# Kernel optimization log

Measured on AMD Instinct MI355X. Metric: run time of the kernel, lower is better.

Reference implementation:

```python
import jax, jax.numpy as jnp
import numpy as np

B, N, D, H = 32, 64, 256, 256
WORD_NUM, REL_NUM, POS_NUM, CAT_NUM = 50000, 50, 48, 5


def setup_inputs() -> dict:
    key = jax.random.key(0)
    ks = jax.random.split(key, 20)
    rng = np.random.default_rng(0)
    # valid dependency trees: head[i] < i, head[0] = -1 (root)
    heads_np = np.zeros((B, N), dtype=np.int32)
    for b in range(B):
        heads_np[b, 0] = -1
        for i in range(1, N):
            heads_np[b, i] = rng.integers(0, i)
    p = lambda k, shape: (0.02 * jax.random.normal(k, shape)).astype(jnp.float32)
    z = lambda shape: jnp.zeros(shape, jnp.float32)
    return {
        "xs": jax.random.randint(ks[0], (B, N), 0, WORD_NUM),
        "heads": jnp.asarray(heads_np),
        "rels": jax.random.randint(ks[1], (B, N), 0, REL_NUM),
        "labels": jax.random.randint(ks[2], (B, N), 0, WORD_NUM),
        "poss": jax.random.randint(ks[3], (B, N), 0, POS_NUM),
        "xlengths": jnp.full((B,), N, dtype=jnp.int32),
        "target_start": jnp.zeros((B,), jnp.int32),
        "target_end": jnp.full((B,), N - 1, jnp.int32),
        "x_mask": jnp.ones((B, N), jnp.float32),
        # parameters
        "emb_W": p(ks[4], (WORD_NUM, D)),
        "rel_W": p(ks[5], (REL_NUM, D)),
        "gru_Wi_f": p(ks[6], (2 * D, 3 * H)), "gru_Wh_f": p(ks[7], (H, 3 * H)),
        "gru_bi_f": z((3 * H,)), "gru_bh_f": z((3 * H,)),
        "gru_Wi_b": p(ks[8], (2 * D, 3 * H)), "gru_Wh_b": p(ks[9], (H, 3 * H)),
        "gru_bi_b": z((3 * H,)), "gru_bh_b": z((3 * H,)),
        "Wt": p(ks[10], (2 * H, D)), "bt": z((D,)),
        "dt_Wx": p(ks[11], (2 * D, 3 * H)), "dt_Uh": p(ks[12], (H, 3 * H)), "dt_b": z((3 * H,)),
        "td_Wx": p(ks[13], (2 * D, 3 * H)), "td_Uh": p(ks[14], (H, 3 * H)), "td_b": z((3 * H,)),
        "fc_W": p(ks[15], (2 * H, 100)), "fc_b": z((100,)),
        "fc2_W": p(ks[16], (100, CAT_NUM)), "fc2_b": z((CAT_NUM,)),
    }


def _gru_cell(xpt, hprev, Uh, bh):
    gh = hprev @ Uh + bh
    xr, xz, xn = jnp.split(xpt, 3, axis=-1)
    hr, hz, hn = jnp.split(gh, 3, axis=-1)
    r = jax.nn.sigmoid(xr + hr)
    zg = jax.nn.sigmoid(xz + hz)
    n = jnp.tanh(xn + r * hn)
    return (1.0 - zg) * n + zg * hprev


def _gru_dir(x, Wi, Wh, bi, bh):
    # x: [B,N,2D] -> hidden sequence [B,N,H]
    xp = x @ Wi + bi  # precompute input projections
    def step(h, xpt):
        hnew = _gru_cell(xpt, h, Wh, bh)
        return hnew, hnew
    h0 = jnp.zeros((x.shape[0], Wh.shape[0]), x.dtype)
    _, hs = jax.lax.scan(step, h0, jnp.swapaxes(xp, 0, 1))
    return jnp.swapaxes(hs, 0, 1)


def _dt_tree(inputs, heads, Wx, Uh, b):
    # bottom-up (child-sum) tree GRU; heads[b,i] < i so reversed order is topological
    Bn, Nn, _ = inputs.shape
    Hh = Uh.shape[0]
    xp = inputs @ Wx + b
    bar = jnp.arange(Bn)
    def step(carry, idx):
        C, Hout = carry  # C: accumulated child hidden sums [B,N,H]
        h = _gru_cell(xp[:, idx], C[:, idx], Uh, jnp.zeros((3 * Hh,), inputs.dtype))
        Hout = Hout.at[:, idx].set(h)
        par = heads[:, idx]
        valid = par >= 0
        C = C.at[bar, jnp.where(valid, par, 0)].add(jnp.where(valid[:, None], h, 0.0))
        return (C, Hout), None
    H0 = jnp.zeros((Bn, Nn, Hh), inputs.dtype)
    (_, Hout), _ = jax.lax.scan(step, (H0, H0), jnp.arange(Nn - 1, -1, -1))
    return Hout


def _td_tree(inputs, heads, Wx, Uh, b):
    # top-down tree GRU: parent hidden flows to children; index order 0..N-1 is topological
    Bn, Nn, _ = inputs.shape
    Hh = Uh.shape[0]
    xp = inputs @ Wx + b
    bar = jnp.arange(Bn)
    def step(Hout, idx):
        par = heads[:, idx]
        valid = par >= 0
        hp = jnp.where(valid[:, None], Hout[bar, jnp.where(valid, par, 0)], 0.0)
        h = _gru_cell(xp[:, idx], hp, Uh, jnp.zeros((3 * Hh,), inputs.dtype))
        Hout = Hout.at[:, idx].set(h)
        return Hout, None
    H0 = jnp.zeros((Bn, Nn, Hh), inputs.dtype)
    Hout, _ = jax.lax.scan(step, H0, jnp.arange(Nn))
    return Hout


def reference(xs, heads, rels, labels, poss, xlengths, target_start, target_end, x_mask,
              emb_W, rel_W,
              gru_Wi_f, gru_Wh_f, gru_bi_f, gru_bh_f,
              gru_Wi_b, gru_Wh_b, gru_bi_b, gru_bh_b,
              Wt, bt, dt_Wx, dt_Uh, dt_b, td_Wx, td_Uh, td_b,
              fc_W, fc_b, fc2_W, fc2_b):
    word_emb = emb_W[xs]
    label_emb = emb_W[labels]  # original uses self.embedding for labels too
    emb = jnp.concatenate([word_emb, label_emb], axis=-1)  # [B,N,2D]
    fwd = _gru_dir(emb, gru_Wi_f, gru_Wh_f, gru_bi_f, gru_bh_f)
    bwd = jnp.flip(_gru_dir(jnp.flip(emb, 1), gru_Wi_b, gru_Wh_b, gru_bi_b, gru_bh_b), 1)
    grus = jnp.concatenate([fwd, bwd], axis=-1) @ Wt + bt  # transform -> [B,N,D]
    rel_emb = rel_W[rels]
    outputs = jnp.concatenate([grus, rel_emb], axis=-1)  # [B,N,2D]
    dt_out = _dt_tree(outputs, heads, dt_Wx, dt_Uh, dt_b)
    td_out = _td_tree(outputs, heads, td_Wx, td_Uh, td_b)
    ctx = jnp.concatenate([dt_out, td_out], axis=-1)  # [B,N,2H]
    ctx = jnp.max(ctx, axis=1)  # max_pool1d over length -> [B,2H]
    ctx = ctx @ fc_W + fc_b
    ctx = ctx @ fc2_W + fc2_b
    return ctx
```

## Files before the change

### kernel.cpp

```cpp
#include <hip/hip_runtime.h>


typedef _Float16 half2v __attribute__((ext_vector_type(2)));
typedef _Float16 half8 __attribute__((ext_vector_type(8)));
typedef unsigned int u32x32 __attribute__((ext_vector_type(32)));
typedef float f32x4v __attribute__((ext_vector_type(4)));

__device__ __forceinline__ float fdot2f(unsigned a, unsigned b, float c) {
#if __has_builtin(__builtin_amdgcn_fdot2)
  return __builtin_amdgcn_fdot2(__builtin_bit_cast(half2v, a),
                                __builtin_bit_cast(half2v, b), c, false);
#else
  half2v av = __builtin_bit_cast(half2v, a), bv = __builtin_bit_cast(half2v, b);
  return c + (float)av.x * (float)bv.x + (float)av.y * (float)bv.y;
#endif
}

__device__ __forceinline__ unsigned packh2(float x, float y) {
  half2v p;
  p.x = (_Float16)x;
  p.y = (_Float16)y;
  return __builtin_bit_cast(unsigned, p);
}
__device__ __forceinline__ unsigned short f2u(float x) {
  return __builtin_bit_cast(unsigned short, (_Float16)x);
}
__device__ __forceinline__ float sigm(float x) { return 1.f / (1.f + __expf(-x)); }
__device__ __forceinline__ float tanh_fast(float x) {
  float cx = fminf(fmaxf(x, -15.f), 15.f);
  float e = __expf(2.f * cx);
  return (e - 1.f) / (e + 1.f);
}

__global__ __launch_bounds__(256) void pack_w(const float* __restrict__ W0,
                                              const float* __restrict__ W1,
                                              const float* __restrict__ W2,
                                              const float* __restrict__ W3, unsigned* P0,
                                              unsigned* P1, unsigned* P2, unsigned* P3) {
  const float* W;
  unsigned* P;
  switch (blockIdx.y) {
    case 0: W = W0; P = P0; break;
    case 1: W = W1; P = P1; break;
    case 2: W = W2; P = P2; break;
    default: W = W3; P = P3; break;
  }
  const int tid = blockIdx.x * 256 + threadIdx.x;
  const int i = tid & 3;
  const int u4 = tid >> 2;
  const int jg = u4 & 127;
  const int d4q = u4 >> 7;
  const int d4 = d4q % 48;
  const int q2 = d4q / 48;
  const int col2 = d4 / 24;
  const int rr = d4 % 24;
  const int g = rr >> 3;
  const int p4 = rr & 7;
  const int kp = p4 * 4 + i;
  const int k = q2 * 64 + kp * 2;
  const int col = g * 256 + col2 * 128 + jg;
  P[tid] = packh2(W[(size_t)k * 768 + col], W[(size_t)(k + 1) * 768 + col]);
}

__global__ __launch_bounds__(256) void tsplit2(const float* __restrict__ W0,
                                               const float* __restrict__ W1,
                                               unsigned short* __restrict__ H0,
                                               unsigned short* __restrict__ L0,
                                               unsigned short* __restrict__ H1,
                                               unsigned short* __restrict__ L1, int K,
                                               int N) {
  const float* __restrict__ W = blockIdx.z ? W1 : W0;
  unsigned short* __restrict__ WThi = blockIdx.z ? H1 : H0;
  unsigned short* __restrict__ WTlo = blockIdx.z ? L1 : L0;
  __shared__ float T[32][33];
  const int ky = blockIdx.y * 32, nx = blockIdx.x * 32;
  const int r = threadIdx.x >> 3, c4 = (threadIdx.x & 7) * 4;
  float4 v = *(const float4*)(W + (size_t)(ky + r) * N + nx + c4);
  T[r][c4 + 0] = v.x;
  T[r][c4 + 1] = v.y;
  T[r][c4 + 2] = v.z;
  T[r][c4 + 3] = v.w;
  __syncthreads();
  float f[4] = {T[c4 + 0][r], T[c4 + 1][r], T[c4 + 2][r], T[c4 + 3][r]};
  ushort4 oh, ol;
  {
    _Float16 h0 = (_Float16)f[0], h1 = (_Float16)f[1], h2 = (_Float16)f[2],
             h3 = (_Float16)f[3];
    oh.x = __builtin_bit_cast(unsigned short, h0);
    oh.y = __builtin_bit_cast(unsigned short, h1);
    oh.z = __builtin_bit_cast(unsigned short, h2);
    oh.w = __builtin_bit_cast(unsigned short, h3);
    ol.x = f2u(f[0] - (float)h0);
    ol.y = f2u(f[1] - (float)h1);
    ol.z = f2u(f[2] - (float)h2);
    ol.w = f2u(f[3] - (float)h3);
  }
  *(ushort4*)(WThi + (size_t)(nx + r) * K + ky + c4) = oh;
  *(ushort4*)(WTlo + (size_t)(nx + r) * K + ky + c4) = ol;
}

__global__ void gather_emb_hl(const int* __restrict__ xs, const int* __restrict__ labels,
                              const float* __restrict__ embW,
                              unsigned short* __restrict__ eHi,
                              unsigned short* __restrict__ eLo) {
  const int row = blockIdx.x, t = threadIdx.x;
  const float4* W4 = (const float4*)embW;
  const int src = (t < 64) ? xs[row] : labels[row];
  float4 v = W4[(size_t)src * 64 + (t & 63)];
  float f[4] = {v.x, v.y, v.z, v.w};
  ushort4 oh, ol;
  _Float16 h0 = (_Float16)f[0], h1 = (_Float16)f[1], h2 = (_Float16)f[2],
           h3 = (_Float16)f[3];
  oh.x = __builtin_bit_cast(unsigned short, h0);
  oh.y = __builtin_bit_cast(unsigned short, h1);
  oh.z = __builtin_bit_cast(unsigned short, h2);
  oh.w = __builtin_bit_cast(unsigned short, h3);
  ol.x = f2u(f[0] - (float)h0);
  ol.y = f2u(f[1] - (float)h1);
  ol.z = f2u(f[2] - (float)h2);
  ol.w = f2u(f[3] - (float)h3);
  const size_t idx = (size_t)row * 512 + (t >> 6) * 256 + (t & 63) * 4;
  *(ushort4*)(eHi + idx) = oh;
  *(ushort4*)(eLo + idx) = ol;
}

__global__ void gather_rel_hl(const int* __restrict__ rels,
                              const float* __restrict__ relW,
                              unsigned short* __restrict__ oHi,
                              unsigned short* __restrict__ oLo) {
  const int row = blockIdx.x, t = threadIdx.x;
  const float4* W4 = (const float4*)relW;
  float4 v = W4[(size_t)rels[row] * 64 + t];
  float f[4] = {v.x, v.y, v.z, v.w};
  ushort4 oh, ol;
  _Float16 h0 = (_Float16)f[0], h1 = (_Float16)f[1], h2 = (_Float16)f[2],
           h3 = (_Float16)f[3];
  oh.x = __builtin_bit_cast(unsigned short, h0);
  oh.y = __builtin_bit_cast(unsigned short, h1);
  oh.z = __builtin_bit_cast(unsigned short, h2);
  oh.w = __builtin_bit_cast(unsigned short, h3);
  ol.x = f2u(f[0] - (float)h0);
  ol.y = f2u(f[1] - (float)h1);
  ol.z = f2u(f[2] - (float)h2);
  ol.w = f2u(f[3] - (float)h3);
  const size_t idx = (size_t)row * 512 + 256 + t * 4;
  *(ushort4*)(oHi + idx) = oh;
  *(ushort4*)(oLo + idx) = ol;
}

__global__ __launch_bounds__(256) void mm16p2(
    const unsigned short* __restrict__ Ahi, const unsigned short* __restrict__ Alo,
    const unsigned short* __restrict__ B0h, const unsigned short* __restrict__ B0l,
    const float* __restrict__ bias0, float* __restrict__ C0,
    const unsigned short* __restrict__ B1h, const unsigned short* __restrict__ B1l,
    const float* __restrict__ bias1, float* __restrict__ C1, int ldc) {
  const unsigned short* __restrict__ Bhi = blockIdx.z ? B1h : B0h;
  const unsigned short* __restrict__ Blo = blockIdx.z ? B1l : B0l;
  const float* __restrict__ bias = blockIdx.z ? bias1 : bias0;
  float* __restrict__ Cf = blockIdx.z ? C1 : C0;
  __shared__ __align__(16) _Float16 As_h[64][40], As_l[64][40];
  __shared__ __align__(16) _Float16 Bs_h[64][40], Bs_l[64][40];
  const int t = threadIdx.x, l = t & 63, w = t >> 6;
  const int bm = blockIdx.y * 64, bn = blockIdx.x * 64;
  const int sr = t >> 2, sc = (t & 3) * 8;
  f32x4v ac0 = {0.f, 0.f, 0.f, 0.f}, ac1 = ac0, ac2 = ac0, ac3 = ac0;
  const int fr = w * 16 + (l & 15), fc = (l >> 4) * 8, lo16 = l & 15;
  for (int kt = 0; kt < 512; kt += 32) {
    *(uint4*)(&As_h[sr][sc]) = *(const uint4*)(Ahi + (size_t)(bm + sr) * 512 + kt + sc);
    *(uint4*)(&As_l[sr][sc]) = *(const uint4*)(Alo + (size_t)(bm + sr) * 512 + kt + sc);
    *(uint4*)(&Bs_h[sr][sc]) = *(const uint4*)(Bhi + (size_t)(bn + sr) * 512 + kt + sc);
    *(uint4*)(&Bs_l[sr][sc]) = *(const uint4*)(Blo + (size_t)(bn + sr) * 512 + kt + sc);
    __syncthreads();
    half8 avh = __builtin_bit_cast(half8, *(const uint4*)(&As_h[fr][fc]));
    half8 avl = __builtin_bit_cast(half8, *(const uint4*)(&As_l[fr][fc]));
#define BH(NT) __builtin_bit_cast(half8, *(const uint4*)(&Bs_h[(NT)*16 + lo16][fc]))
#define BL(NT) __builtin_bit_cast(half8, *(const uint4*)(&Bs_l[(NT)*16 + lo16][fc]))
    half8 b0h = BH(0), b1h = BH(1), b2h = BH(2), b3h = BH(3);
    half8 b0l = BL(0), b1l = BL(1), b2l = BL(2), b3l = BL(3);
#undef BH
#undef BL
    ac0 = __builtin_amdgcn_mfma_f32_16x16x32_f16(avh, b0h, ac0, 0, 0, 0);
    ac1 = __builtin_amdgcn_mfma_f32_16x16x32_f16(avh, b1h, ac1, 0, 0, 0);
    ac2 = __builtin_amdgcn_mfma_f32_16x16x32_f16(avh, b2h, ac2, 0, 0, 0);
    ac3 = __builtin_amdgcn_mfma_f32_16x16x32_f16(avh, b3h, ac3, 0, 0, 0);
    ac0 = __builtin_amdgcn_mfma_f32_16x16x32_f16(avh, b0l, ac0, 0, 0, 0);
    ac1 = __builtin_amdgcn_mfma_f32_16x16x32_f16(avh, b1l, ac1, 0, 0, 0);
    ac2 = __builtin_amdgcn_mfma_f32_16x16x32_f16(avh, b2l, ac2, 0, 0, 0);
    ac3 = __builtin_amdgcn_mfma_f32_16x16x32_f16(avh, b3l, ac3, 0, 0, 0);
    ac0 = __builtin_amdgcn_mfma_f32_16x16x32_f16(avl, b0h, ac0, 0, 0, 0);
    ac1 = __builtin_amdgcn_mfma_f32_16x16x32_f16(avl, b1h, ac1, 0, 0, 0);
    ac2 = __builtin_amdgcn_mfma_f32_16x16x32_f16(avl, b2h, ac2, 0, 0, 0);
    ac3 = __builtin_amdgcn_mfma_f32_16x16x32_f16(avl, b3h, ac3, 0, 0, 0);
    __syncthreads();
  }
  const int hi4 = l >> 4;
#define EPI(AC, NT)                                                            \
  {                                                                            \
    _Pragma("unroll") for (int i = 0; i < 4; ++i) {                            \
      const int row = bm + w * 16 + hi4 * 4 + i;                               \
      const int col = bn + (NT)*16 + lo16;                                     \
      Cf[(size_t)row * ldc + col] = (AC)[i] + bias[col];                       \
    }                                                                          \
  }
  EPI(ac0, 0) EPI(ac1, 1) EPI(ac2, 2) EPI(ac3, 3)
#undef EPI
}

__global__ __launch_bounds__(256) void mm16s_wt(const float* __restrict__ A,
                                                const float* __restrict__ W,
                                                const float* __restrict__ bias,
                                                unsigned short* __restrict__ CHi,
                                                unsigned short* __restrict__ CLo, int N,
                                                int ldc) {
  __shared__ __align__(16) _Float16 Ahi[64][40], Alo[64][40];
  __shared__ __align__(16) _Float16 Bhi[64][40], Blo[64][40];
  const int t = threadIdx.x, l = t & 63, w = t >> 6;
  const int bm = blockIdx.y * 64, bn = blockIdx.x * 64;
  const int ar = t >> 2, ac8 = (t & 3) * 8;
  const int bk = t >> 3, bn8 = (t & 7) * 8;
  f32x4v ac0 = {0.f, 0.f, 0.f, 0.f}, ac1 = ac0, ac2 = ac0, ac3 = ac0;
  const int fr = w * 16 + (l & 15), fc = (l >> 4) * 8, lo16 = l & 15;
  for (int kt = 0; kt < 512; kt += 32) {
    {
      const float* ap = A + (size_t)(bm + ar) * 512 + kt + ac8;
      float4 v0 = *(const float4*)ap;
      float4 v1 = *(const float4*)(ap + 4);
      float av[8] = {v0.x, v0.y, v0.z, v0.w, v1.x, v1.y, v1.z, v1.w};
#pragma unroll
      for (int i = 0; i < 8; ++i) {
        _Float16 h = (_Float16)av[i];
        Ahi[ar][ac8 + i] = h;
        Alo[ar][ac8 + i] = (_Float16)(av[i] - (float)h);
      }
    }
    {
      const float* wp = W + (size_t)(kt + bk) * N + bn + bn8;
      float4 v0 = *(const float4*)wp;
      float4 v1 = *(const float4*)(wp + 4);
      float wv[8] = {v0.x, v0.y, v0.z, v0.w, v1.x, v1.y, v1.z, v1.w};
#pragma unroll
      for (int i = 0; i < 8; ++i) {
        _Float16 h = (_Float16)wv[i];
        Bhi[bn8 + i][bk] = h;
        Blo[bn8 + i][bk] = (_Float16)(wv[i] - (float)h);
      }
    }
    __syncthreads();
    half8 avh = __builtin_bit_cast(half8, *(const uint4*)(&Ahi[fr][fc]));
    half8 avl = __builtin_bit_cast(half8, *(const uint4*)(&Alo[fr][fc]));
#define BH(NT) __builtin_bit_cast(half8, *(const uint4*)(&Bhi[(NT)*16 + lo16][fc]))
#define BL(NT) __builtin_bit_cast(half8, *(const uint4*)(&Blo[(NT)*16 + lo16][fc]))
    half8 b0h = BH(0), b1h = BH(1), b2h = BH(2), b3h = BH(3);
    half8 b0l = BL(0), b1l = BL(1), b2l = BL(2), b3l = BL(3);
#undef BH
#undef BL
    ac0 = __builtin_amdgcn_mfma_f32_16x16x32_f16(avh, b0h, ac0, 0, 0, 0);
    ac1 = __builtin_amdgcn_mfma_f32_16x16x32_f16(avh, b1h, ac1, 0, 0, 0);
    ac2 = __builtin_amdgcn_mfma_f32_16x16x32_f16(avh, b2h, ac2, 0, 0, 0);
    ac3 = __builtin_amdgcn_mfma_f32_16x16x32_f16(avh, b3h, ac3, 0, 0, 0);
    ac0 = __builtin_amdgcn_mfma_f32_16x16x32_f16(avh, b0l, ac0, 0, 0, 0);
    ac1 = __builtin_amdgcn_mfma_f32_16x16x32_f16(avh, b1l, ac1, 0, 0, 0);
    ac2 = __builtin_amdgcn_mfma_f32_16x16x32_f16(avh, b2l, ac2, 0, 0, 0);
    ac3 = __builtin_amdgcn_mfma_f32_16x16x32_f16(avh, b3l, ac3, 0, 0, 0);
    ac0 = __builtin_amdgcn_mfma_f32_16x16x32_f16(avl, b0h, ac0, 0, 0, 0);
    ac1 = __builtin_amdgcn_mfma_f32_16x16x32_f16(avl, b1h, ac1, 0, 0, 0);
    ac2 = __builtin_amdgcn_mfma_f32_16x16x32_f16(avl, b2h, ac2, 0, 0, 0);
    ac3 = __builtin_amdgcn_mfma_f32_16x16x32_f16(avl, b3h, ac3, 0, 0, 0);
    __syncthreads();
  }
  const int hi4 = l >> 4;
#define EPI(AC, NT)                                                            \
  {                                                                            \
    _Pragma("unroll") for (int i = 0; i < 4; ++i) {                            \
      const int row = bm + w * 16 + hi4 * 4 + i;                               \
      const int col = bn + (NT)*16 + lo16;                                     \
      float v = (AC)[i] + bias[col];                                           \
      _Float16 h = (_Float16)v;                                                \
      CHi[(size_t)row * ldc + col] = __builtin_bit_cast(unsigned short, h);    \
      CLo[(size_t)row * ldc + col] = f2u(v - (float)h);                        \
    }                                                                          \
  }
  EPI(ac0, 0) EPI(ac1, 1) EPI(ac2, 2) EPI(ac3, 3)
#undef EPI
}

template <int NP>
__device__ __forceinline__ void stage_w(const uint4* __restrict__ P4, int q2, int jg,
                                        int t, uint2 (*Wl)[512], u32x32& w0, u32x32& w1,
                                        u32x32& w2) {
#pragma unroll
  for (int p4 = 0; p4 < 8; ++p4) {
    uint4 v0 = P4[(q2 * 48 + p4) * 128 + jg];
    w0[4 * p4 + 0] = v0.x; w0[4 * p4 + 1] = v0.y;
    w0[4 * p4 + 2] = v0.z; w0[4 * p4 + 3] = v0.w;
    uint4 v1 = P4[(q2 * 48 + 8 + p4) * 128 + jg];
    w1[4 * p4 + 0] = v1.x; w1[4 * p4 + 1] = v1.y;
    w1[4 * p4 + 2] = v1.z; w1[4 * p4 + 3] = v1.w;
    uint4 v2 = P4[(q2 * 48 + 16 + p4) * 128 + jg];
    w2[4 * p4 + 0] = v2.x; w2[4 * p4 + 1] = v2.y;
    w2[4 * p4 + 2] = v2.z; w2[4 * p4 + 3] = v2.w;
  }
#pragma unroll
  for (int g = 0; g < 3; ++g)
#pragma unroll
    for (int p4 = 0; p4 < NP; ++p4) {
      uint4 v = P4[(q2 * 48 + 24 + g * 8 + p4) * 128 + jg];
      Wl[(g * NP + p4) * 2 + 0][t] = make_uint2(v.x, v.y);
      Wl[(g * NP + p4) * 2 + 1][t] = make_uint2(v.z, v.w);
    }
}

template <int NP>
__device__ __forceinline__ void dot_step(const u32x32& w0, const u32x32& w1,
                                         const u32x32& w2, const uint2 (*Wl)[512], int t,
                                         const uint4* __restrict__ P4, int sb,
                                         const uint4* hv4, float& a0, float& a1,
                                         float& a2, float& a3, float& a4, float& a5) {
#pragma unroll
  for (int c = 0; c < 8; ++c) {
    uint4 hu = hv4[c];
    a0 = fdot2f(w0[4 * c + 0], hu.x, a0); a0 = fdot2f(w0[4 * c + 1], hu.y, a0);
    a0 = fdot2f(w0[4 * c + 2], hu.z, a0); a0 = fdot2f(w0[4 * c + 3], hu.w, a0);
    a1 = fdot2f(w1[4 * c + 0], hu.x, a1); a1 = fdot2f(w1[4 * c + 1], hu.y, a1);
    a1 = fdot2f(w1[4 * c + 2], hu.z, a1); a1 = fdot2f(w1[4 * c + 3], hu.w, a1);
    a2 = fdot2f(w2[4 * c + 0], hu.x, a2); a2 = fdot2f(w2[4 * c + 1], hu.y, a2);
    a2 = fdot2f(w2[4 * c + 2], hu.z, a2); a2 = fdot2f(w2[4 * c + 3], hu.w, a2);
    if (c < NP) {
      uint2 u0 = Wl[(0 * NP + c) * 2 + 0][t], u1 = Wl[(0 * NP + c) * 2 + 1][t];
      a3 = fdot2f(u0.x, hu.x, a3); a3 = fdot2f(u0.y, hu.y, a3);
      a3 = fdot2f(u1.x, hu.z, a3); a3 = fdot2f(u1.y, hu.w, a3);
      uint2 v0 = Wl[(1 * NP + c) * 2 + 0][t], v1 = Wl[(1 * NP + c) * 2 + 1][t];
      a4 = fdot2f(v0.x, hu.x, a4); a4 = fdot2f(v0.y, hu.y, a4);
      a4 = fdot2f(v1.x, hu.z, a4); a4 = fdot2f(v1.y, hu.w, a4);
      uint2 x0 = Wl[(2 * NP + c) * 2 + 0][t], x1 = Wl[(2 * NP + c) * 2 + 1][t];
      a5 = fdot2f(x0.x, hu.x, a5); a5 = fdot2f(x0.y, hu.y, a5);
      a5 = fdot2f(x1.x, hu.z, a5); a5 = fdot2f(x1.y, hu.w, a5);
    } else {
      uint4 s0 = P4[sb + (0 * 8 + c) * 128];
      a3 = fdot2f(s0.x, hu.x, a3); a3 = fdot2f(s0.y, hu.y, a3);
      a3 = fdot2f(s0.z, hu.z, a3); a3 = fdot2f(s0.w, hu.w, a3);
      uint4 s1 = P4[sb + (1 * 8 + c) * 128];
      a4 = fdot2f(s1.x, hu.x, a4); a4 = fdot2f(s1.y, hu.y, a4);
      a4 = fdot2f(s1.z, hu.z, a4); a4 = fdot2f(s1.w, hu.w, a4);
      uint4 s2 = P4[sb + (2 * 8 + c) * 128];
      a5 = fdot2f(s2.x, hu.x, a5); a5 = fdot2f(s2.y, hu.y, a5);
      a5 = fdot2f(s2.z, hu.z, a5); a5 = fdot2f(s2.w, hu.w, a5);
    }
  }
}

__global__ __launch_bounds__(512) void gru_scan_h(
    const unsigned* __restrict__ Pf, const unsigned* __restrict__ Pb,
    const float* __restrict__ bh_f, const float* __restrict__ bh_b,
    const float* __restrict__ xp_f, const float* __restrict__ xp_b,
    float* __restrict__ grus) {
  const int b = blockIdx.x & 31, dir = blockIdx.x >> 5;
  const uint4* __restrict__ P4 = (const uint4*)(dir ? Pb : Pf);
  const float* __restrict__ bh = dir ? bh_b : bh_f;
  const float* __restrict__ xp = dir ? xp_b : xp_f;

  __shared__ uint2 Wl[36][512];
  __shared__ float part[4][3][256];
  __shared__ __align__(16) unsigned h2[128];

  const int t = threadIdx.x, jg = t & 127, q2 = t >> 7;
  const int sb = (q2 * 48 + 24) * 128 + jg;

  u32x32 w0, w1, w2;
  stage_w<6>(P4, q2, jg, t, Wl, w0, w1, w2);

  float br0 = 0.f, br1 = 0.f, bz0 = 0.f, bz1 = 0.f, bn0 = 0.f, bn1 = 0.f;
  float hp0 = 0.f, hp1 = 0.f;
  if (t < 128) {
    br0 = bh[2 * t];       br1 = bh[2 * t + 1];
    bz0 = bh[256 + 2 * t]; bz1 = bh[256 + 2 * t + 1];
    bn0 = bh[512 + 2 * t]; bn1 = bh[512 + 2 * t + 1];
    h2[t] = 0u;
  }
  __syncthreads();

  for (int s = 0; s < 64; ++s) {
    const int nn = dir ? (63 - s) : s;
    float2 pxr, pxz, pxn;
    if (t < 128) {
      const float* xrow = xp + (size_t)(b * 64 + nn) * 768;
      pxr = *(const float2*)(xrow + 2 * t);
      pxz = *(const float2*)(xrow + 256 + 2 * t);
      pxn = *(const float2*)(xrow + 512 + 2 * t);
    }
    float a0 = 0.f, a1 = 0.f, a2 = 0.f, a3 = 0.f, a4 = 0.f, a5 = 0.f;
    dot_step<6>(w0, w1, w2, Wl, t, P4, sb, (const uint4*)(h2 + q2 * 32), a0, a1, a2, a3,
                a4, a5);
    part[q2][0][jg] = a0;
    part[q2][0][128 + jg] = a3;
    part[q2][1][jg] = a1;
    part[q2][1][128 + jg] = a4;
    part[q2][2][jg] = a2;
    part[q2][2][128 + jg] = a5;
    __syncthreads();
    if (t < 128) {
      float s0r = 0, s1r = 0, s0z = 0, s1z = 0, s0n = 0, s1n = 0;
#pragma unroll
      for (int q = 0; q < 4; ++q) {
        float2 pr = *(const float2*)(&part[q][0][2 * t]); s0r += pr.x; s1r += pr.y;
        float2 pz = *(const float2*)(&part[q][1][2 * t]); s0z += pz.x; s1z += pz.y;
        float2 pn = *(const float2*)(&part[q][2][2 * t]); s0n += pn.x; s1n += pn.y;
      }
      float r0 = sigm(pxr.x + s0r + br0), r1 = sigm(pxr.y + s1r + br1);
      float z0 = sigm(pxz.x + s0z + bz0), z1 = sigm(pxz.y + s1z + bz1);
      float n0 = tanh_fast(pxn.x + r0 * (s0n + bn0));
      float n1 = tanh_fast(pxn.y + r1 * (s1n + bn1));
      float h0 = (1.f - z0) * n0 + z0 * hp0;
      float h1 = (1.f - z1) * n1 + z1 * hp1;
      hp0 = h0;
      hp1 = h1;
      h2[t] = packh2(h0, h1);
      float2 o;
      o.x = h0;
      o.y = h1;
      *(float2*)(grus + (size_t)(b * 64 + nn) * 512 + dir * 256 + 2 * t) = o;
    }
    __syncthreads();
  }
}

__global__ __launch_bounds__(512) void tree_scan_g(
    const unsigned* __restrict__ Pdt, const unsigned* __restrict__ Ptd,
    const float* __restrict__ xp_dt, const float* __restrict__ xp_td,
    const int* __restrict__ heads, float* __restrict__ ctx, float* __restrict__ Sg) {
  const int b = blockIdx.x & 31, istd = blockIdx.x >> 5;
  const uint4* __restrict__ P4 = (const uint4*)(istd ? Ptd : Pdt);
  const float* __restrict__ xp = istd ? xp_td : xp_dt;
  float* __restrict__ S = Sg + (size_t)blockIdx.x * 16384;

  __shared__ __align__(16) unsigned S2[65][128];
  __shared__ uint2 Wl[24][512];
  __shared__ float part[4][3][256];
  __shared__ int hd[64];

  const int t = threadIdx.x, jg = t & 127, q2 = t >> 7;
  const int sb = (q2 * 48 + 24) * 128 + jg;

  u32x32 w0, w1, w2;
  stage_w<4>(P4, q2, jg, t, Wl, w0, w1, w2);

  for (int i = t; i < 16384; i += 512) S[i] = 0.f;
  for (int i = t; i < 65 * 128; i += 512) (&S2[0][0])[i] = 0u;
  if (t < 64) hd[t] = heads[b * 64 + t];
  __syncthreads();

  float mx0 = -1e30f, mx1 = -1e30f;

  for (int s = 0; s < 64; ++s) {
    const int idx = istd ? s : (63 - s);
    const int par = hd[idx];
    const int srow = istd ? (par >= 0 ? par : 64) : idx;

    float2 pxr, pxz, pxn;
    float hp0 = 0.f, hp1 = 0.f, acc0 = 0.f, acc1 = 0.f;
    if (t < 128) {
      const float* xrow = xp + (size_t)(b * 64 + idx) * 768;
      pxr = *(const float2*)(xrow + 2 * t);
      pxz = *(const float2*)(xrow + 256 + 2 * t);
      pxn = *(const float2*)(xrow + 512 + 2 * t);
      if (istd) {
        if (par >= 0) {
          float2 v = *(const float2*)(S + par * 256 + 2 * t);
          hp0 = v.x;
          hp1 = v.y;
        }
      } else {
        float2 v = *(const float2*)(S + idx * 256 + 2 * t);
        hp0 = v.x;
        hp1 = v.y;
        if (par >= 0) {
          float2 a = *(const float2*)(S + par * 256 + 2 * t);
          acc0 = a.x;
          acc1 = a.y;
        }
      }
    }
    float a0 = 0.f, a1 = 0.f, a2 = 0.f, a3 = 0.f, a4 = 0.f, a5 = 0.f;
    dot_step<4>(w0, w1, w2, Wl, t, P4, sb, (const uint4*)(&S2[srow][q2 * 32]), a0, a1,
                a2, a3, a4, a5);
    part[q2][0][jg] = a0;
    part[q2][0][128 + jg] = a3;
    part[q2][1][jg] = a1;
    part[q2][1][128 + jg] = a4;
    part[q2][2][jg] = a2;
    part[q2][2][128 + jg] = a5;
    __syncthreads();
    if (t < 128) {
      float s0r = 0, s1r = 0, s0z = 0, s1z = 0, s0n = 0, s1n = 0;
#pragma unroll
      for (int q = 0; q < 4; ++q) {
        float2 pr = *(const float2*)(&part[q][0][2 * t]); s0r += pr.x; s1r += pr.y;
        float2 pz = *(const float2*)(&part[q][1][2 * t]); s0z += pz.x; s1z += pz.y;
        float2 pn = *(const float2*)(&part[q][2][2 * t]); s0n += pn.x; s1n += pn.y;
      }
      float r0 = sigm(pxr.x + s0r), r1 = sigm(pxr.y + s1r);
      float z0 = sigm(pxz.x + s0z), z1 = sigm(pxz.y + s1z);
      float n0 = tanh_fast(pxn.x + r0 * s0n), n1 = tanh_fast(pxn.y + r1 * s1n);
      float h0 = (1.f - z0) * n0 + z0 * hp0;
      float h1 = (1.f - z1) * n1 + z1 * hp1;
      mx0 = fmaxf(mx0, h0);
      mx1 = fmaxf(mx1, h1);
      if (istd) {
        float2 o;
        o.x = h0;
        o.y = h1;
        *(float2*)(S + idx * 256 + 2 * t) = o;
        S2[idx][t] = packh2(h0, h1);
      } else if (par >= 0) {
        float c0 = acc0 + h0;
        float c1 = acc1 + h1;
        float2 o;
        o.x = c0;
        o.y = c1;
        *(float2*)(S + par * 256 + 2 * t) = o;
        S2[par][t] = packh2(c0, c1);
      }
    }
    __syncthreads();
  }

  if (t < 128) {
    float2 o;
    o.x = mx0;
    o.y = mx1;
    *(float2*)(ctx + (size_t)b * 512 + istd * 256 + 2 * t) = o;
  }
}

__global__ __launch_bounds__(128) void final_k(const float* __restrict__ ctx_g,
                                               const float* __restrict__ fcW,
                                               const float* __restrict__ fcb,
                                               const float* __restrict__ fc2W,
                                               const float* __restrict__ fc2b,
                                               float* __restrict__ out) {
  const int b = blockIdx.x, t = threadIdx.x;
  __shared__ float ctx[512];
  __shared__ float f1[100];
  for (int i = t; i < 512; i += 128) ctx[i] = ctx_g[(size_t)b * 512 + i];
  __syncthreads();
  if (t < 100) {
    float a = fcb[t];
    for (int k = 0; k < 512; ++k) a = fmaf(ctx[k], fcW[k * 100 + t], a);
    f1[t] = a;
  }
  __syncthreads();
  if (t < 5) {
    float a = fc2b[t];
    for (int k = 0; k < 100; ++k) a = fmaf(f1[k], fc2W[k * 5 + t], a);
    out[b * 5 + t] = a;
  }
}

extern "C" void kernel_launch(void* const* d_in, const int* in_sizes, int n_in, void* d_out,
                              int out_size, void* d_ws, size_t ws_size, hipStream_t stream) {
  const int* xs = (const int*)d_in[0];
  const int* heads = (const int*)d_in[1];
  const int* rels = (const int*)d_in[2];
  const int* labels = (const int*)d_in[3];
  const float* emb_W = (const float*)d_in[9];
  const float* rel_W = (const float*)d_in[10];
  const float* Wi_f = (const float*)d_in[11];
  const float* Wh_f = (const float*)d_in[12];
  const float* bi_f = (const float*)d_in[13];
  const float* bh_f = (const float*)d_in[14];
  const float* Wi_b = (const float*)d_in[15];
  const float* Wh_b = (const float*)d_in[16];
  const float* bi_b = (const float*)d_in[17];
  const float* bh_b = (const float*)d_in[18];
  const float* Wt = (const float*)d_in[19];
  const float* bt = (const float*)d_in[20];
  const float* dt_Wx = (const float*)d_in[21];
  const float* dt_Uh = (const float*)d_in[22];
  const float* dt_b = (const float*)d_in[23];
  const float* td_Wx = (const float*)d_in[24];
  const float* td_Uh = (const float*)d_in[25];
  const float* td_b = (const float*)d_in[26];
  const float* fc_W = (const float*)d_in[27];
  const float* fc_b = (const float*)d_in[28];
  const float* fc2_W = (const float*)d_in[29];
  const float* fc2_b = (const float*)d_in[30];

  float* ws = (float*)d_ws;
  float* xp_f = ws;
  float* xp_b = ws + 1572864;
  float* grus = ws + 3145728;
  float* ctx = ws + 4194304;
  unsigned* P0 = (unsigned*)(ws + 4210688);
  unsigned* P1 = P0 + 98304;
  unsigned* P2 = P1 + 98304;
  unsigned* P3 = P2 + 98304;
  unsigned short* embHi = (unsigned short*)(ws + 4603904);
  unsigned short* embLo = (unsigned short*)(ws + 5128192);
  unsigned short* WTh_a = (unsigned short*)(ws + 5652480);
  unsigned short* WTl_a = (unsigned short*)(ws + 5849088);
  unsigned short* WTh_b = (unsigned short*)(ws + 6045696);
  unsigned short* WTl_b = (unsigned short*)(ws + 6242304);
  unsigned short* outHi = embHi;
  unsigned short* outLo = embLo;
  float* Sg = ws + 4603904;

  pack_w<<<dim3(384, 4), 256, 0, stream>>>(Wh_f, Wh_b, dt_Uh, td_Uh, P0, P1, P2, P3);
  tsplit2<<<dim3(24, 16, 2), 256, 0, stream>>>(Wi_f, Wi_b, WTh_a, WTl_a, WTh_b, WTl_b,
                                               512, 768);
  gather_emb_hl<<<2048, 128, 0, stream>>>(xs, labels, emb_W, embHi, embLo);
  mm16p2<<<dim3(12, 32, 2), 256, 0, stream>>>(embHi, embLo, WTh_a, WTl_a, bi_f, xp_f,
                                              WTh_b, WTl_b, bi_b, xp_b, 768);
  gru_scan_h<<<64, 512, 0, stream>>>(P0, P1, bh_f, bh_b, xp_f, xp_b, grus);
  tsplit2<<<dim3(24, 16, 2), 256, 0, stream>>>(dt_Wx, td_Wx, WTh_a, WTl_a, WTh_b, WTl_b,
                                               512, 768);
  mm16s_wt<<<dim3(4, 32), 256, 0, stream>>>(grus, Wt, bt, outHi, outLo, 256, 512);
  gather_rel_hl<<<2048, 64, 0, stream>>>(rels, rel_W, outHi, outLo);
  mm16p2<<<dim3(12, 32, 2), 256, 0, stream>>>(outHi, outLo, WTh_a, WTl_a, dt_b, xp_f,
                                              WTh_b, WTl_b, td_b, xp_b, 768);
  tree_scan_g<<<64, 512, 0, stream>>>(P2, P3, xp_f, xp_b, heads, ctx, Sg);
  final_k<<<32, 128, 0, stream>>>(ctx, fc_W, fc_b, fc2_W, fc2_b, (float*)d_out);
}
```

Before: 299.8 us.

## Replace LDS partial-sum reduction with wave shuffles in GRU and tree scans

The thread-to-column mapping in both recurrent scan kernels is remapped so that the four K-quarter partial sums for a column sit in the same wavefront (lanes 16 apart). The partials are then combined with xor-shuffles instead of going through a shared 'part' array and an extra barrier. The GRU scan also double-buffers its hidden state so each step needs only one __syncthreads. This shortens the serial per-step critical path, at the cost of 6×2 shuffles per step. The gate math is now spread over 16 lanes per wave rather than the first 128 threads, and global and LDS stores become scalar rather than float2.

Measured after the change: 340.0 us. 1.13x slower.

```diff
diff --git a/kernel.cpp b/kernel.cpp
--- a/kernel.cpp
+++ b/kernel.cpp
@@ -31,6 +31,10 @@
   float e = __expf(2.f * cx);
   return (e - 1.f) / (e + 1.f);
 }
+
+#define RED2(v)                                                                \
+  v += __shfl_xor(v, 16);                                                      \
+  v += __shfl_xor(v, 32);
 
 __global__ __launch_bounds__(256) void pack_w(const float* __restrict__ W0,
                                               const float* __restrict__ W1,
@@ -349,7 +353,7 @@
   }
 }
 
-__global__ __launch_bounds__(512) void gru_scan_h(
+__global__ __launch_bounds__(512) void gru_scan_w(
     const unsigned* __restrict__ Pf, const unsigned* __restrict__ Pb,
     const float* __restrict__ bh_f, const float* __restrict__ bh_b,
     const float* __restrict__ xp_f, const float* __restrict__ xp_b,
@@ -360,71 +364,64 @@
   const float* __restrict__ xp = dir ? xp_b : xp_f;
 
   __shared__ uint2 Wl[36][512];
-  __shared__ float part[4][3][256];
-  __shared__ __align__(16) unsigned h2[128];
-
-  const int t = threadIdx.x, jg = t & 127, q2 = t >> 7;
+  __shared__ __align__(16) unsigned h2[2][128];
+
+  const int t = threadIdx.x;
+  const int lane = t & 63, wv = t >> 6;
+  const int q2 = lane >> 4;
+  const int jg = (lane & 15) + wv * 16;
   const int sb = (q2 * 48 + 24) * 128 + jg;
 
   u32x32 w0, w1, w2;
   stage_w<6>(P4, q2, jg, t, Wl, w0, w1, w2);
 
-  float br0 = 0.f, br1 = 0.f, bz0 = 0.f, bz1 = 0.f, bn0 = 0.f, bn1 = 0.f;
-  float hp0 = 0.f, hp1 = 0.f;
-  if (t < 128) {
-    br0 = bh[2 * t];       br1 = bh[2 * t + 1];
-    bz0 = bh[256 + 2 * t]; bz1 = bh[256 + 2 * t + 1];
-    bn0 = bh[512 + 2 * t]; bn1 = bh[512 + 2 * t + 1];
-    h2[t] = 0u;
-  }
+  const bool actv = (q2 == 0);
+  float br0 = 0, bz0 = 0, bn0 = 0, br1 = 0, bz1 = 0, bn1 = 0;
+  float hc0 = 0.f, hc1 = 0.f;
+  if (actv) {
+    br0 = bh[jg];       bz0 = bh[256 + jg]; bn0 = bh[512 + jg];
+    br1 = bh[128 + jg]; bz1 = bh[384 + jg]; bn1 = bh[640 + jg];
+  }
+  if (t < 256) ((unsigned*)h2)[t] = 0u;
   __syncthreads();
 
   for (int s = 0; s < 64; ++s) {
     const int nn = dir ? (63 - s) : s;
-    float2 pxr, pxz, pxn;
-    if (t < 128) {
-      const float* xrow = xp + (size_t)(b * 64 + nn) * 768;
-      pxr = *(const float2*)(xrow + 2 * t);
-      pxz = *(const float2*)(xrow + 256 + 2 * t);
-      pxn = *(const float2*)(xrow + 512 + 2 * t);
+    const int rb = s & 1;
+    float x0, x1, x2, x3, x4, x5;
+    if (actv) {
+      const float* xr = xp + (size_t)(b * 64 + nn) * 768;
+      x0 = xr[jg];       x1 = xr[256 + jg]; x2 = xr[512 + jg];
+      x3 = xr[128 + jg]; x4 = xr[384 + jg]; x5 = xr[640 + jg];
     }
     float a0 = 0.f, a1 = 0.f, a2 = 0.f, a3 = 0.f, a4 = 0.f, a5 = 0.f;
-    dot_step<6>(w0, w1, w2, Wl, t, P4, sb, (const uint4*)(h2 + q2 * 32), a0, a1, a2, a3,
-                a4, a5);
-    part[q2][0][jg] = a0;
-    part[q2][0][128 + jg] = a3;
-    part[q2][1][jg] = a1;
-    part[q2][1][128 + jg] = a4;
-    part[q2][2][jg] = a2;
-    part[q2][2][128 + jg] = a5;
+    dot_step<6>(w0, w1, w2, Wl, t, P4, sb, (const uint4*)(&h2[rb][q2 * 32]), a0, a1, a2,
+                a3, a4, a5);
+    RED2(a0) RED2(a1) RED2(a2) RED2(a3) RED2(a4) RED2(a5)
+    if (actv) {
+      {
+        float r = sigm(x0 + a0 + br0), z = sigm(x1 + a1 + bz0);
+        float n = tanh_fast(x2 + r * (a2 + bn0));
+        hc0 = (1.f - z) * n + z * hc0;
+      }
+      {
+        float r = sigm(x3 + a3 + br1), z = sigm(x4 + a4 + bz1);
+        float n = tanh_fast(x5 + r * (a5 + bn1));
+        hc1 = (1.f - z) * n + z * hc1;
+      }
+      grus[(size_t)(b * 64 + nn) * 512 + dir * 256 + jg] = hc0;
+      grus[(size_t)(b * 64 + nn) * 512 + dir * 256 + 128 + jg] = hc1;
+      float p0 = __shfl_xor(hc0, 1), p1 = __shfl_xor(hc1, 1);
+      if ((jg & 1) == 0) {
+        h2[rb ^ 1][jg >> 1] = packh2(hc0, p0);
+        h2[rb ^ 1][64 + (jg >> 1)] = packh2(hc1, p1);
+      }
+    }
     __syncthreads();
-    if (t < 128) {
-      float s0r = 0, s1r = 0, s0z = 0, s1z = 0, s0n = 0, s1n = 0;
-#pragma unroll
-      for (int q = 0; q < 4; ++q) {
-        float2 pr = *(const float2*)(&part[q][0][2 * t]); s0r += pr.x; s1r += pr.y;
-        float2 pz = *(const float2*)(&part[q][1][2 * t]); s0z += pz.x; s1z += pz.y;
-        float2 pn = *(const float2*)(&part[q][2][2 * t]); s0n += pn.x; s1n += pn.y;
-      }
-      float r0 = sigm(pxr.x + s0r + br0), r1 = sigm(pxr.y + s1r + br1);
-      float z0 = sigm(pxz.x + s0z + bz0), z1 = sigm(pxz.y + s1z + bz1);
-      float n0 = tanh_fast(pxn.x + r0 * (s0n + bn0));
-      float n1 = tanh_fast(pxn.y + r1 * (s1n + bn1));
-      float h0 = (1.f - z0) * n0 + z0 * hp0;
-      float h1 = (1.f - z1) * n1 + z1 * hp1;
-      hp0 = h0;
-      hp1 = h1;
-      h2[t] = packh2(h0, h1);
-      float2 o;
-      o.x = h0;
-      o.y = h1;
-      *(float2*)(grus + (size_t)(b * 64 + nn) * 512 + dir * 256 + 2 * t) = o;
-    }
-    __syncthreads();
-  }
-}
-
-__global__ __launch_bounds__(512) void tree_scan_g(
+  }
+}
+
+__global__ __launch_bounds__(512) void tree_scan_w(
     const unsigned* __restrict__ Pdt, const unsigned* __restrict__ Ptd,
     const float* __restrict__ xp_dt, const float* __restrict__ xp_td,
     const int* __restrict__ heads, float* __restrict__ ctx, float* __restrict__ Sg) {
@@ -435,10 +432,12 @@
 
   __shared__ __align__(16) unsigned S2[65][128];
   __shared__ uint2 Wl[24][512];
-  __shared__ float part[4][3][256];
   __shared__ int hd[64];
 
-  const int t = threadIdx.x, jg = t & 127, q2 = t >> 7;
+  const int t = threadIdx.x;
+  const int lane = t & 63, wv = t >> 6;
+  const int q2 = lane >> 4;
+  const int jg = (lane & 15) + wv * 16;
   const int sb = (q2 * 48 + 24) * 128 + jg;
 
   u32x32 w0, w1, w2;
@@ -449,6 +448,7 @@
   if (t < 64) hd[t] = heads[b * 64 + t];
   __syncthreads();
 
+  const bool actv = (q2 == 0);
   float mx0 = -1e30f, mx1 = -1e30f;
 
   for (int s = 0; s < 64; ++s) {
@@ -456,79 +456,69 @@
     const int par = hd[idx];
     const int srow = istd ? (par >= 0 ? par : 64) : idx;
 
-    float2 pxr, pxz, pxn;
+    float x0, x1, x2, x3, x4, x5;
     float hp0 = 0.f, hp1 = 0.f, acc0 = 0.f, acc1 = 0.f;
-    if (t < 128) {
-      const float* xrow = xp + (size_t)(b * 64 + idx) * 768;
-      pxr = *(const float2*)(xrow + 2 * t);
-      pxz = *(const float2*)(xrow + 256 + 2 * t);
-      pxn = *(const float2*)(xrow + 512 + 2 * t);
+    if (actv) {
+      const float* xr = xp + (size_t)(b * 64 + idx) * 768;
+      x0 = xr[jg];       x1 = xr[256 + jg]; x2 = xr[512 + jg];
+      x3 = xr[128 + jg]; x4 = xr[384 + jg]; x5 = xr[640 + jg];
       if (istd) {
         if (par >= 0) {
-          float2 v = *(const float2*)(S + par * 256 + 2 * t);
-          hp0 = v.x;
-          hp1 = v.y;
+          hp0 = S[par * 256 + jg];
+          hp1 = S[par * 256 + 128 + jg];
         }
       } else {
-        float2 v = *(const float2*)(S + idx * 256 + 2 * t);
-        hp0 = v.x;
-        hp1 = v.y;
+        hp0 = S[idx * 256 + jg];
+        hp1 = S[idx * 256 + 128 + jg];
         if (par >= 0) {
-          float2 a = *(const float2*)(S + par * 256 + 2 * t);
-          acc0 = a.x;
-          acc1 = a.y;
+          acc0 = S[par * 256 + jg];
+          acc1 = S[par * 256 + 128 + jg];
         }
       }
     }
     float a0 = 0.f, a1 = 0.f, a2 = 0.f, a3 = 0.f, a4 = 0.f, a5 = 0.f;
     dot_step<4>(w0, w1, w2, Wl, t, P4, sb, (const uint4*)(&S2[srow][q2 * 32]), a0, a1,
                 a2, a3, a4, a5);
-    part[q2][0][jg] = a0;
-    part[q2][0][128 + jg] = a3;
-    part[q2][1][jg] = a1;
-    part[q2][1][128 + jg] = a4;
-    part[q2][2][jg] = a2;
-    part[q2][2][128 + jg] = a5;
-    __syncthreads();
-    if (t < 128) {
-      float s0r = 0, s1r = 0, s0z = 0, s1z = 0, s0n = 0, s1n = 0;
-#pragma unroll
-      for (int q = 0; q < 4; ++q) {
-        float2 pr = *(const float2*)(&part[q][0][2 * t]); s0r += pr.x; s1r += pr.y;
-        float2 pz = *(const float2*)(&part[q][1][2 * t]); s0z += pz.x; s1z += pz.y;
-        float2 pn = *(const float2*)(&part[q][2][2 * t]); s0n += pn.x; s1n += pn.y;
-      }
-      float r0 = sigm(pxr.x + s0r), r1 = sigm(pxr.y + s1r);
-      float z0 = sigm(pxz.x + s0z), z1 = sigm(pxz.y + s1z);
-      float n0 = tanh_fast(pxn.x + r0 * s0n), n1 = tanh_fast(pxn.y + r1 * s1n);
-      float h0 = (1.f - z0) * n0 + z0 * hp0;
-      float h1 = (1.f - z1) * n1 + z1 * hp1;
+    RED2(a0) RED2(a1) RED2(a2) RED2(a3) RED2(a4) RED2(a5)
+    if (actv) {
+      float h0, h1;
+      {
+        float r = sigm(x0 + a0), z = sigm(x1 + a1);
+        float n = tanh_fast(x2 + r * a2);
+        h0 = (1.f - z) * n + z * hp0;
+      }
+      {
+        float r = sigm(x3 + a3), z = sigm(x4 + a4);
+        float n = tanh_fast(x5 + r * a5);
+        h1 = (1.f - z) * n + z * hp1;
+      }
       mx0 = fmaxf(mx0, h0);
       mx1 = fmaxf(mx1, h1);
       if (istd) {
-        float2 o;
-        o.x = h0;
-        o.y = h1;
-        *(float2*)(S + idx * 256 + 2 * t) = o;
-        S2[idx][t] = packh2(h0, h1);
+        S[idx * 256 + jg] = h0;
+        S[idx * 256 + 128 + jg] = h1;
+        float p0 = __shfl_xor(h0, 1), p1 = __shfl_xor(h1, 1);
+        if ((jg & 1) == 0) {
+          S2[idx][jg >> 1] = packh2(h0, p0);
+          S2[idx][64 + (jg >> 1)] = packh2(h1, p1);
+        }
       } else if (par >= 0) {
-        float c0 = acc0 + h0;
-        float c1 = acc1 + h1;
-        float2 o;
-        o.x = c0;
-        o.y = c1;
-        *(float2*)(S + par * 256 + 2 * t) = o;
-        S2[par][t] = packh2(c0, c1);
+        float c0 = acc0 + h0, c1 = acc1 + h1;
+        S[par * 256 + jg] = c0;
+        S[par * 256 + 128 + jg] = c1;
+        float p0 = __shfl_xor(c0, 1), p1 = __shfl_xor(c1, 1);
+        if ((jg & 1) == 0) {
+          S2[par][jg >> 1] = packh2(c0, p0);
+          S2[par][64 + (jg >> 1)] = packh2(c1, p1);
+        }
       }
     }
     __syncthreads();
   }
 
-  if (t < 128) {
-    float2 o;
-    o.x = mx0;
-    o.y = mx1;
-    *(float2*)(ctx + (size_t)b * 512 + istd * 256 + 2 * t) = o;
+  if (actv) {
+    ctx[(size_t)b * 512 + istd * 256 + jg] = mx0;
+    ctx[(size_t)b * 512 + istd * 256 + 128 + jg] = mx1;
   }
 }
 
@@ -610,13 +600,13 @@
   gather_emb_hl<<<2048, 128, 0, stream>>>(xs, labels, emb_W, embHi, embLo);
   mm16p2<<<dim3(12, 32, 2), 256, 0, stream>>>(embHi, embLo, WTh_a, WTl_a, bi_f, xp_f,
                                               WTh_b, WTl_b, bi_b, xp_b, 768);
-  gru_scan_h<<<64, 512, 0, stream>>>(P0, P1, bh_f, bh_b, xp_f, xp_b, grus);
+  gru_scan_w<<<64, 512, 0, stream>>>(P0, P1, bh_f, bh_b, xp_f, xp_b, grus);
   tsplit2<<<dim3(24, 16, 2), 256, 0, stream>>>(dt_Wx, td_Wx, WTh_a, WTl_a, WTh_b, WTl_b,
                                                512, 768);
   mm16s_wt<<<dim3(4, 32), 256, 0, stream>>>(grus, Wt, bt, outHi, outLo, 256, 512);
   gather_rel_hl<<<2048, 64, 0, stream>>>(rels, rel_W, outHi, outLo);
   mm16p2<<<dim3(12, 32, 2), 256, 0, stream>>>(outHi, outLo, WTh_a, WTl_a, dt_b, xp_f,
                                               WTh_b, WTl_b, td_b, xp_b, 768);
-  tree_scan_g<<<64, 512, 0, stream>>>(P2, P3, xp_f, xp_b, heads, ctx, Sg);
+  tree_scan_w<<<64, 512, 0, stream>>>(P2, P3, xp_f, xp_b, heads, ctx, Sg);
   final_k<<<32, 128, 0, stream>>>(ctx, fc_W, fc_b, fc2_W, fc2_b, (float*)d_out);
 }
```
